# Kernel tuning notes

Hardware: AMD Instinct MI355X
Metric: run time of the kernel (lower is better)

Reference implementation:

```python
import jax, jax.numpy as jnp
import numpy as np

NEG_INF = -1e30


def _rotate_half(t):
    d = t.shape[-1] // 2
    t1, t2 = t[..., :d], t[..., d:]
    return jnp.concatenate([-t2, t1], axis=-1)


def _apply_rope(t, cos, sin):
    # t: [B, H, T, D]; cos/sin: [T, D] broadcast over B, H
    return t * cos[None, None, :, :] + _rotate_half(t) * sin[None, None, :, :]


def setup_inputs() -> dict:
    key = jax.random.key(0)
    ks = jax.random.split(key, 5)
    B, T, C, H = 2, 2048, 2048, 16
    D = C // H
    x = jax.random.normal(ks[0], (B, T, C), dtype=jnp.float32)
    # RoPE tables (realistic: derived from inv freqs)
    inv_freq = 1.0 / (10000.0 ** (jnp.arange(0, D, 2, dtype=jnp.float32) / D))
    freqs = jnp.arange(T, dtype=jnp.float32)[:, None] * inv_freq[None, :]
    emb = jnp.concatenate([freqs, freqs], axis=-1)  # [T, D]
    cos, sin = jnp.cos(emb), jnp.sin(emb)
    W_attn = jax.random.normal(ks[1], (C, 3 * C), dtype=jnp.float32) * (1.0 / np.sqrt(C))
    W_proj = jax.random.normal(ks[2], (C, C), dtype=jnp.float32) * (1.0 / np.sqrt(C))
    return {"x": x, "cos": cos, "sin": sin, "W_attn": W_attn, "W_proj": W_proj}


def reference(x, cos, sin, W_attn, W_proj):
    B, T, C = x.shape
    H = 16
    D = C // H
    qkv = x @ W_attn  # [B, T, 3C]
    q, k, v = jnp.split(qkv, 3, axis=-1)
    # [B, T, C] -> [B, H, T, D]
    to_heads = lambda t: t.reshape(B, T, H, D).transpose(0, 2, 1, 3)
    q, k, v = to_heads(q), to_heads(k), to_heads(v)
    q = _apply_rope(q, cos, sin)
    k = _apply_rope(k, cos, sin)
    scale = 1.0 / np.sqrt(D).astype(np.float32)
    scores = jnp.einsum("bhqd,bhkd->bhqk", q, k) * scale
    causal = jnp.tril(jnp.ones((T, T), dtype=bool))
    scores = jnp.where(causal[None, None, :, :], scores, NEG_INF)
    attn = jax.nn.softmax(scores, axis=-1)
    out = jnp.einsum("bhqk,bhkd->bhqd", attn, v)  # [B, H, T, D]
    out = out.transpose(0, 2, 1, 3).reshape(B, T, C)
    return out @ W_proj
```

## Files before the change

### kernel.cpp

```cpp
#include <hip/hip_runtime.h>
#include <stdint.h>

#define Bc   2
#define Tc   2048
#define Cc   2048
#define Hc   16
#define Dc   128
#define BT   4096
#define N3   6144
#define QSCALE 0.08838834764831845f

typedef _Float16 f16x8 __attribute__((ext_vector_type(8)));
typedef _Float16 f16x4 __attribute__((ext_vector_type(4)));
typedef float    f32x4 __attribute__((ext_vector_type(4)));

__device__ __forceinline__ void gload_lds16(const void* g, void* l) {
  __builtin_amdgcn_global_load_lds(
      (__attribute__((address_space(1))) void*)(uintptr_t)g,
      (__attribute__((address_space(3))) void*)(unsigned int)(uintptr_t)l,
      16, 0, 0);
}

__global__ __launch_bounds__(256) void cvt_f16_kernel(const float* __restrict__ in,
                                                      _Float16* __restrict__ out, int n4) {
  int i = blockIdx.x * 256 + threadIdx.x;
  if (i < n4) {
    float4 v = ((const float4*)in)[i];
    f16x4 o; o[0]=(_Float16)v.x; o[1]=(_Float16)v.y; o[2]=(_Float16)v.z; o[3]=(_Float16)v.w;
    ((f16x4*)out)[i] = o;
  }
}

__global__ __launch_bounds__(256) void transpose_cvt_kernel(const float* __restrict__ W,
                                                            _Float16* __restrict__ Wt,
                                                            int K, int N) {
  const int n0 = blockIdx.x * 64, k0 = blockIdx.y * 64;
  __shared__ float tile[64][65];
  const int tid = threadIdx.x;
  #pragma unroll
  for (int i = 0; i < 4; ++i) {
    int u = i * 256 + tid, r = u >> 4, s = u & 15;
    float4 v = *(const float4*)&W[(size_t)(k0 + r) * N + n0 + s * 4];
    tile[r][s*4+0] = v.x; tile[r][s*4+1] = v.y; tile[r][s*4+2] = v.z; tile[r][s*4+3] = v.w;
  }
  __syncthreads();
  #pragma unroll
  for (int i = 0; i < 2; ++i) {
    int u = i * 256 + tid, c = u >> 3, rg = u & 7;
    f16x8 o;
    #pragma unroll
    for (int j = 0; j < 8; ++j) o[j] = (_Float16)tile[rg * 8 + j][c];
    *(f16x8*)&Wt[(size_t)(n0 + c) * K + k0 + rg * 8] = o;
  }
}

template<bool OUT16>
__global__ __launch_bounds__(256) void gemm_bt_kernel(const _Float16* __restrict__ A,
                                                      const _Float16* __restrict__ Bt,
                                                      void* __restrict__ C,
                                                      int M, int N, int K) {
  const int tid = threadIdx.x;
  const int w = tid >> 6, lane = tid & 63, g = lane >> 4, c16 = lane & 15;
  const int m0 = blockIdx.y * 128, n0 = blockIdx.x * 128;
  const int wm = (w >> 1) * 64, wn = (w & 1) * 64;

  __shared__ __align__(16) _Float16 Alds[128 * 32];
  __shared__ __align__(16) _Float16 Blds[128 * 32];

  const int r4 = lane >> 2, k8 = (lane & 3) * 8;
  const char* aSrc = (const char*)(A + (size_t)(m0 + r4) * K + k8);
  const char* bSrc = (const char*)(Bt + (size_t)(n0 + r4) * K + k8);

  f32x4 acc[4][4] = {};

  for (int k0 = 0; k0 < K; k0 += 32) {
    __syncthreads();
    #pragma unroll
    for (int j = 0; j < 2; ++j) {
      int ch = j * 4 + w;
      gload_lds16(aSrc + ((size_t)ch * 16 * K + k0) * 2, (char*)Alds + ch * 1024);
      gload_lds16(bSrc + ((size_t)ch * 16 * K + k0) * 2, (char*)Blds + ch * 1024);
    }
    __syncthreads();
    f16x8 af[4], bf[4];
    #pragma unroll
    for (int i = 0; i < 4; ++i) {
      af[i] = *(const f16x8*)&Alds[(wm + i * 16 + c16) * 32 + g * 8];
      bf[i] = *(const f16x8*)&Blds[(wn + i * 16 + c16) * 32 + g * 8];
    }
    #pragma unroll
    for (int mi = 0; mi < 4; ++mi)
      #pragma unroll
      for (int ni = 0; ni < 4; ++ni)
        acc[mi][ni] = __builtin_amdgcn_mfma_f32_16x16x32_f16(af[mi], bf[ni], acc[mi][ni], 0, 0, 0);
  }

  #pragma unroll
  for (int mi = 0; mi < 4; ++mi)
    #pragma unroll
    for (int ni = 0; ni < 4; ++ni) {
      int row = m0 + wm + mi * 16 + g * 4;
      int col = n0 + wn + ni * 16 + c16;
      #pragma unroll
      for (int r = 0; r < 4; ++r) {
        if constexpr (OUT16) ((_Float16*)C)[(size_t)(row + r) * N + col] = (_Float16)acc[mi][ni][r];
        else                 ((float*)C)[(size_t)(row + r) * N + col]    = acc[mi][ni][r];
      }
    }
}

__global__ __launch_bounds__(256) void rope_qk_kernel(const _Float16* __restrict__ qkv,
                                                      const float* __restrict__ cosT,
                                                      const float* __restrict__ sinT,
                                                      _Float16* __restrict__ Qr,
                                                      _Float16* __restrict__ Kr) {
  const int bt = blockIdx.x;
  const int b = bt >> 11, t = bt & 2047;
  const int tid = threadIdx.x;
  const _Float16* row = qkv + (size_t)bt * N3;
  const int sw = (t & 7) * 8;
  #pragma unroll
  for (int i = 0; i < 4; ++i) {
    int p = i * 256 + tid;
    int h = p >> 6, d = p & 63;
    float cs = cosT[t * Dc + d], sn = sinT[t * Dc + d];
    float ql = (float)row[h * Dc + d],        qh = (float)row[h * Dc + d + 64];
    float kl = (float)row[Cc + h * Dc + d],   kh = (float)row[Cc + h * Dc + d + 64];
    float q0 = ql * cs - qh * sn, q1 = qh * cs + ql * sn;
    float k0 = kl * cs - kh * sn, k1 = kh * cs + kl * sn;
    size_t obase = ((size_t)(b * Hc + h) * Tc + t) * Dc;
    Qr[obase + d]        = (_Float16)(q0 * QSCALE);
    Qr[obase + d + 64]   = (_Float16)(q1 * QSCALE);
    Kr[obase + (d ^ sw)]        = (_Float16)k0;
    Kr[obase + ((d + 64) ^ sw)] = (_Float16)k1;
  }
}

__global__ __launch_bounds__(256) void vtrans_kernel(const _Float16* __restrict__ qkv,
                                                     _Float16* __restrict__ Vt) {
  const int t0 = blockIdx.x * 64, d0 = blockIdx.y * 64, bh = blockIdx.z;
  const int b = bh >> 4, h = bh & 15;
  __shared__ __align__(16) _Float16 tile[64][72];
  const int tid = threadIdx.x;
  #pragma unroll
  for (int i = 0; i < 2; ++i) {
    int u = i * 256 + tid, tr = u >> 3, sg = u & 7;
    f16x8 v = *(const f16x8*)&qkv[((size_t)b * Tc + t0 + tr) * N3 + 2 * Cc + h * Dc + d0 + sg * 8];
    *(f16x8*)&tile[tr][sg * 8] = v;
  }
  __syncthreads();
  #pragma unroll
  for (int i = 0; i < 2; ++i) {
    int u = i * 256 + tid, dl = u >> 3, tg = u & 7;
    int d = d0 + dl;
    f16x8 o;
    #pragma unroll
    for (int j = 0; j < 8; ++j) o[j] = tile[tg * 8 + j][dl];
    size_t off = ((size_t)bh * Dc + d) * Tc + t0 + ((tg ^ (d & 7)) * 8);
    *(f16x8*)&Vt[off] = o;
  }
}

__global__ __launch_bounds__(256, 2) void attn_kernel(const _Float16* __restrict__ Qr,
                                                      const _Float16* __restrict__ Kr,
                                                      const _Float16* __restrict__ Vt,
                                                      _Float16* __restrict__ Oh) {
  const int bh = blockIdx.x;
  const int pr = blockIdx.y;
  const int qtA = pr, qtB = 31 - pr;
  const int tid = threadIdx.x;
  const int w = tid >> 6, lane = tid & 63, g = lane >> 4, c16 = lane & 15, l7 = lane & 7;
  const int rA = qtA * 64 + w * 16;
  const int rB = qtB * 64 + w * 16;

  __shared__ __align__(16) _Float16 Klds[2][64 * 128];
  __shared__ __align__(16) _Float16 Vlds[2][128 * 64];
  __shared__ __align__(16) _Float16 Plds[4][16][72];

  const _Float16* Qb = Qr + (size_t)bh * Tc * Dc;
  f16x8 qfA[4], qfB[4];
  #pragma unroll
  for (int kb = 0; kb < 4; ++kb) {
    qfA[kb] = *(const f16x8*)&Qb[(size_t)(rA + c16) * Dc + kb * 32 + g * 8];
    qfB[kb] = *(const f16x8*)&Qb[(size_t)(rB + c16) * Dc + kb * 32 + g * 8];
  }

  f32x4 accA[8] = {}, accB[8] = {};
  float mA[4], lA[4], mB[4], lB[4];
  #pragma unroll
  for (int r = 0; r < 4; ++r) { mA[r] = -1e30f; lA[r] = 0.f; mB[r] = -1e30f; lB[r] = 0.f; }

  const _Float16* Kt0 = Kr + (size_t)bh * Tc * Dc;

  auto stage = [&](int j, int buf) {
    const char* src = (const char*)(Kt0 + (size_t)j * 64 * Dc);
    #pragma unroll
    for (int i = 0; i < 4; ++i) {
      int ch = i * 4 + w;
      gload_lds16(src + ch * 1024 + lane * 16, (char*)(&Klds[buf][0]) + ch * 1024);
    }
    #pragma unroll
    for (int i = 0; i < 4; ++i) {
      int ch = i * 4 + w;
      int d = ch * 8 + (lane >> 3);
      const char* gs = (const char*)(Vt + ((size_t)bh * Dc + d) * Tc + j * 64) + (lane & 7) * 16;
      gload_lds16(gs, (char*)(&Vlds[buf][0]) + ch * 1024);
    }
  };

  auto process_tile = [&](f32x4* s, f32x4* acc, float* m, float* l,
                          int rT, int j, int cur, bool maskit) {
    if (maskit) {
      #pragma unroll
      for (int ni = 0; ni < 4; ++ni)
        #pragma unroll
        for (int r = 0; r < 4; ++r) {
          int q = rT + g * 4 + r;
          int kv = j * 64 + ni * 16 + c16;
          if (kv > q) s[ni][r] = -1e30f;
        }
    }
    #pragma unroll
    for (int r = 0; r < 4; ++r) {
      float mt = fmaxf(fmaxf(s[0][r], s[1][r]), fmaxf(s[2][r], s[3][r]));
      #pragma unroll
      for (int off = 1; off < 16; off <<= 1) mt = fmaxf(mt, __shfl_xor(mt, off));
      float mnew = fmaxf(m[r], mt);
      float alpha = __expf(m[r] - mnew);
      float p0 = __expf(s[0][r] - mnew), p1 = __expf(s[1][r] - mnew);
      float p2 = __expf(s[2][r] - mnew), p3 = __expf(s[3][r] - mnew);
      float ls = p0 + p1 + p2 + p3;
      #pragma unroll
      for (int off = 1; off < 16; off <<= 1) ls += __shfl_xor(ls, off);
      l[r] = l[r] * alpha + ls;
      m[r] = mnew;
      #pragma unroll
      for (int di = 0; di < 8; ++di) acc[di][r] *= alpha;
      int prow = g * 4 + r;
      Plds[w][prow][0  + c16] = (_Float16)p0;
      Plds[w][prow][16 + c16] = (_Float16)p1;
      Plds[w][prow][32 + c16] = (_Float16)p2;
      Plds[w][prow][48 + c16] = (_Float16)p3;
    }
    #pragma unroll
    for (int kvb = 0; kvb < 2; ++kvb) {
      f16x8 pf = *(const f16x8*)&Plds[w][c16][kvb * 32 + g * 8];
      __builtin_amdgcn_s_setprio(1);
      #pragma unroll
      for (int di = 0; di < 8; ++di) {
        f16x8 vf = *(const f16x8*)&Vlds[cur][(di * 16 + c16) * 64 + ((kvb * 4 + g) ^ l7) * 8];
        acc[di] = __builtin_amdgcn_mfma_f32_16x16x32_f16(pf, vf, acc[di], 0, 0, 0);
      }
      __builtin_amdgcn_s_setprio(0);
    }
  };

  const int nt = qtB + 1;
  stage(0, 0);
  __syncthreads();
  int cur = 0;
  for (int j = 0; j < nt; ++j) {
    if (j + 1 < nt) stage(j + 1, cur ^ 1);
    const bool doA = (j <= qtA);

    f32x4 sA[4] = {}, sB[4] = {};
    #pragma unroll
    for (int kb = 0; kb < 4; ++kb) {
      f16x8 bfr[4];
      #pragma unroll
      for (int ni = 0; ni < 4; ++ni)
        bfr[ni] = *(const f16x8*)&Klds[cur][(ni * 16 + c16) * 128 + ((kb * 4 + g) ^ l7) * 8];
      __builtin_amdgcn_s_setprio(1);
      #pragma unroll
      for (int ni = 0; ni < 4; ++ni) {
        sB[ni] = __builtin_amdgcn_mfma_f32_16x16x32_f16(qfB[kb], bfr[ni], sB[ni], 0, 0, 0);
        if (doA)
          sA[ni] = __builtin_amdgcn_mfma_f32_16x16x32_f16(qfA[kb], bfr[ni], sA[ni], 0, 0, 0);
      }
      __builtin_amdgcn_s_setprio(0);
    }

    process_tile(sB, accB, mB, lB, rB, j, cur, j == qtB);
    if (doA) process_tile(sA, accA, mA, lA, rA, j, cur, j == qtA);

    __syncthreads();
    cur ^= 1;
  }

  const int b = bh >> 4, h = bh & 15;
  #pragma unroll
  for (int tile = 0; tile < 2; ++tile) {
    f32x4* acc = tile ? accB : accA;
    float* l   = tile ? lB   : lA;
    int rT     = tile ? rB   : rA;
    #pragma unroll
    for (int r = 0; r < 4; ++r) {
      float inv = 1.0f / l[r];
      int trow = rT + g * 4 + r;
      _Float16* orow = Oh + ((size_t)b * Tc + trow) * Cc + h * Dc;
      #pragma unroll
      for (int di = 0; di < 8; ++di)
        orow[di * 16 + c16] = (_Float16)(acc[di][r] * inv);
    }
  }
}

extern "C" void kernel_launch(void* const* d_in, const int* in_sizes, int n_in,
                              void* d_out, int out_size, void* d_ws, size_t ws_size,
                              hipStream_t stream) {
  const float* x      = (const float*)d_in[0];
  const float* cosT   = (const float*)d_in[1];
  const float* sinT   = (const float*)d_in[2];
  const float* W_attn = (const float*)d_in[3];
  const float* W_proj = (const float*)d_in[4];
  float* out = (float*)d_out;

  const size_t OFF_XH   = 0;
  const size_t OFF_WAH  = 16777216;
  const size_t OFF_WPH  = 41943040;
  const size_t OFF_QKV  = 50331648;
  const size_t OFF_QR   = 100663296;
  const size_t OFF_KR   = 117440512;
  const size_t OFF_VT   = 134217728;
  const size_t WS_NEEDED = 150994944;
  if (ws_size < WS_NEEDED) return;

  char* ws = (char*)d_ws;
  _Float16* xh   = (_Float16*)(ws + OFF_XH);
  _Float16* Wah  = (_Float16*)(ws + OFF_WAH);
  _Float16* Wph  = (_Float16*)(ws + OFF_WPH);
  _Float16* qkvh = (_Float16*)(ws + OFF_QKV);
  _Float16* Qr   = (_Float16*)(ws + OFF_QR);
  _Float16* Kr   = (_Float16*)(ws + OFF_KR);
  _Float16* Vt   = (_Float16*)(ws + OFF_VT);
  _Float16* Oh   = qkvh;

  cvt_f16_kernel<<<dim3(8192), dim3(256), 0, stream>>>(x, xh, (Bc * Tc * Cc) / 4);
  transpose_cvt_kernel<<<dim3(N3 / 64, Cc / 64), dim3(256), 0, stream>>>(W_attn, Wah, Cc, N3);
  transpose_cvt_kernel<<<dim3(Cc / 64, Cc / 64), dim3(256), 0, stream>>>(W_proj, Wph, Cc, Cc);
  gemm_bt_kernel<true><<<dim3(N3 / 128, BT / 128), dim3(256), 0, stream>>>(xh, Wah, qkvh, BT, N3, Cc);
  rope_qk_kernel<<<dim3(BT), dim3(256), 0, stream>>>(qkvh, cosT, sinT, Qr, Kr);
  vtrans_kernel<<<dim3(Tc / 64, Dc / 64, Bc * Hc), dim3(256), 0, stream>>>(qkvh, Vt);
  attn_kernel<<<dim3(Bc * Hc, 16), dim3(256), 0, stream>>>(Qr, Kr, Vt, Oh);
  gemm_bt_kernel<false><<<dim3(Cc / 128, BT / 128), dim3(256), 0, stream>>>(Oh, Wph, out, BT, Cc, Cc);
}
```

Before: 447.8 us.

## Replace GEMM with double-buffered 256x128 tile kernel with swizzled LDS

Replaces the single-buffered 128x128 GEMM with a 512-thread kernel computing 256x128 tiles over a K step of 64. Global-to-LDS loads for tile t+2 are issued while tile t is computed, using explicit vmcnt waits. LDS reads use an XOR swizzle to avoid bank conflicts, s_setprio raises MFMA priority, and blocks are remapped across XCDs. It uses 96KB of LDS per block, which limits occupancy, and depends on carefully placed waitcnt and barrier ordering for correctness.

```diff
diff --git a/kernel.cpp b/kernel.cpp
--- a/kernel.cpp
+++ b/kernel.cpp
@@ -54,53 +54,97 @@
   }
 }
 
+#define GLDS_BUF 49152
+
 template<bool OUT16>
-__global__ __launch_bounds__(256) void gemm_bt_kernel(const _Float16* __restrict__ A,
-                                                      const _Float16* __restrict__ Bt,
-                                                      void* __restrict__ C,
-                                                      int M, int N, int K) {
-  const int tid = threadIdx.x;
-  const int w = tid >> 6, lane = tid & 63, g = lane >> 4, c16 = lane & 15;
-  const int m0 = blockIdx.y * 128, n0 = blockIdx.x * 128;
-  const int wm = (w >> 1) * 64, wn = (w & 1) * 64;
-
-  __shared__ __align__(16) _Float16 Alds[128 * 32];
-  __shared__ __align__(16) _Float16 Blds[128 * 32];
-
-  const int r4 = lane >> 2, k8 = (lane & 3) * 8;
-  const char* aSrc = (const char*)(A + (size_t)(m0 + r4) * K + k8);
-  const char* bSrc = (const char*)(Bt + (size_t)(n0 + r4) * K + k8);
+__global__ __launch_bounds__(512, 2) void gemm256_kernel(const _Float16* __restrict__ A,
+                                                         const _Float16* __restrict__ Bt,
+                                                         void* __restrict__ C,
+                                                         int M, int N, int K) {
+  __shared__ __align__(16) char glds[2 * GLDS_BUF];
+  const int tid = threadIdx.x;
+  const int wid = tid >> 6, lane = tid & 63, g = lane >> 4, c16 = lane & 15;
+  const int wr = wid >> 1, wc = wid & 1;
+
+  const int nblocks = gridDim.x, chunk = nblocks >> 3;
+  const int bid = blockIdx.x;
+  const int sw = (bid & 7) * chunk + (bid >> 3);
+  const int ntm = M >> 8;
+  const int m0 = (sw % ntm) * 256, n0 = (sw / ntm) * 128;
+
+  const int ntk = K >> 6;
+  const int row8 = tid >> 3, s8 = tid & 7;
+  const int scol = (s8 ^ (row8 & 7)) * 8;
+  const int swz = (c16 & 7) << 4;
+
+  auto stage_tile = [&](char* bb, int kt) {
+    #pragma unroll
+    for (int c = 0; c < 4; ++c)
+      gload_lds16(A + (size_t)(m0 + c * 64 + row8) * K + kt * 64 + scol,
+                  bb + c * 8192 + tid * 16);
+    #pragma unroll
+    for (int c = 0; c < 2; ++c)
+      gload_lds16(Bt + (size_t)(n0 + c * 64 + row8) * K + kt * 64 + scol,
+                  bb + 32768 + c * 8192 + tid * 16);
+  };
 
   f32x4 acc[4][4] = {};
 
-  for (int k0 = 0; k0 < K; k0 += 32) {
-    __syncthreads();
-    #pragma unroll
-    for (int j = 0; j < 2; ++j) {
-      int ch = j * 4 + w;
-      gload_lds16(aSrc + ((size_t)ch * 16 * K + k0) * 2, (char*)Alds + ch * 1024);
-      gload_lds16(bSrc + ((size_t)ch * 16 * K + k0) * 2, (char*)Blds + ch * 1024);
-    }
-    __syncthreads();
-    f16x8 af[4], bf[4];
-    #pragma unroll
-    for (int i = 0; i < 4; ++i) {
-      af[i] = *(const f16x8*)&Alds[(wm + i * 16 + c16) * 32 + g * 8];
-      bf[i] = *(const f16x8*)&Blds[(wn + i * 16 + c16) * 32 + g * 8];
-    }
+  stage_tile(glds, 0);
+  stage_tile(glds + GLDS_BUF, 1);
+  asm volatile("s_waitcnt vmcnt(6)" ::: "memory");
+  __builtin_amdgcn_s_barrier();
+
+  for (int t = 0; t < ntk; ++t) {
+    char* bb = glds + (t & 1) * GLDS_BUF;
+
+    f16x8 a0[4], b0[4];
     #pragma unroll
     for (int mi = 0; mi < 4; ++mi)
+      a0[mi] = *(const f16x8*)(bb + (wr * 64 + mi * 16 + c16) * 128 + ((g * 16) ^ swz));
+    #pragma unroll
+    for (int ni = 0; ni < 4; ++ni)
+      b0[ni] = *(const f16x8*)(bb + 32768 + (wc * 64 + ni * 16 + c16) * 128 + ((g * 16) ^ swz));
+    __builtin_amdgcn_s_setprio(1);
+    #pragma unroll
+    for (int mi = 0; mi < 4; ++mi)
       #pragma unroll
       for (int ni = 0; ni < 4; ++ni)
-        acc[mi][ni] = __builtin_amdgcn_mfma_f32_16x16x32_f16(af[mi], bf[ni], acc[mi][ni], 0, 0, 0);
+        acc[mi][ni] = __builtin_amdgcn_mfma_f32_16x16x32_f16(a0[mi], b0[ni], acc[mi][ni], 0, 0, 0);
+    __builtin_amdgcn_s_setprio(0);
+
+    f16x8 a1[4], b1[4];
+    #pragma unroll
+    for (int mi = 0; mi < 4; ++mi)
+      a1[mi] = *(const f16x8*)(bb + (wr * 64 + mi * 16 + c16) * 128 + ((64 + g * 16) ^ swz));
+    #pragma unroll
+    for (int ni = 0; ni < 4; ++ni)
+      b1[ni] = *(const f16x8*)(bb + 32768 + (wc * 64 + ni * 16 + c16) * 128 + ((64 + g * 16) ^ swz));
+    asm volatile("s_waitcnt lgkmcnt(0)" ::: "memory");
+    __builtin_amdgcn_sched_barrier(0);
+    __builtin_amdgcn_s_barrier();
+    if (t + 2 < ntk) {
+      stage_tile(bb, t + 2);
+      asm volatile("s_waitcnt vmcnt(6)" ::: "memory");
+    } else if (t + 1 < ntk) {
+      asm volatile("s_waitcnt vmcnt(0)" ::: "memory");
+    }
+    __builtin_amdgcn_s_barrier();
+    __builtin_amdgcn_s_setprio(1);
+    #pragma unroll
+    for (int mi = 0; mi < 4; ++mi)
+      #pragma unroll
+      for (int ni = 0; ni < 4; ++ni)
+        acc[mi][ni] = __builtin_amdgcn_mfma_f32_16x16x32_f16(a1[mi], b1[ni], acc[mi][ni], 0, 0, 0);
+    __builtin_amdgcn_s_setprio(0);
   }
 
   #pragma unroll
   for (int mi = 0; mi < 4; ++mi)
     #pragma unroll
     for (int ni = 0; ni < 4; ++ni) {
-      int row = m0 + wm + mi * 16 + g * 4;
-      int col = n0 + wn + ni * 16 + c16;
+      int row = m0 + wr * 64 + mi * 16 + g * 4;
+      int col = n0 + wc * 64 + ni * 16 + c16;
       #pragma unroll
       for (int r = 0; r < 4; ++r) {
         if constexpr (OUT16) ((_Float16*)C)[(size_t)(row + r) * N + col] = (_Float16)acc[mi][ni][r];
@@ -338,9 +382,9 @@
   cvt_f16_kernel<<<dim3(8192), dim3(256), 0, stream>>>(x, xh, (Bc * Tc * Cc) / 4);
   transpose_cvt_kernel<<<dim3(N3 / 64, Cc / 64), dim3(256), 0, stream>>>(W_attn, Wah, Cc, N3);
   transpose_cvt_kernel<<<dim3(Cc / 64, Cc / 64), dim3(256), 0, stream>>>(W_proj, Wph, Cc, Cc);
-  gemm_bt_kernel<true><<<dim3(N3 / 128, BT / 128), dim3(256), 0, stream>>>(xh, Wah, qkvh, BT, N3, Cc);
+  gemm256_kernel<true><<<dim3((BT / 256) * (N3 / 128)), dim3(512), 0, stream>>>(xh, Wah, qkvh, BT, N3, Cc);
   rope_qk_kernel<<<dim3(BT), dim3(256), 0, stream>>>(qkvh, cosT, sinT, Qr, Kr);
   vtrans_kernel<<<dim3(Tc / 64, Dc / 64, Bc * Hc), dim3(256), 0, stream>>>(qkvh, Vt);
   attn_kernel<<<dim3(Bc * Hc, 16), dim3(256), 0, stream>>>(Qr, Kr, Vt, Oh);
-  gemm_bt_kernel<false><<<dim3(Cc / 128, BT / 128), dim3(256), 0, stream>>>(Oh, Wph, out, BT, Cc, Cc);
-}
+  gemm256_kernel<false><<<dim3((BT / 256) * (Cc / 128)), dim3(512), 0, stream>>>(Oh, Wph, out, BT, Cc, Cc);
+}
```

New measurement: 405.9 us. -9.4%, faster.
